# Kernel optimization log

Hardware: AMD Instinct MI355X
Metric: run time of the kernel (lower is better)

## Reference

```python
import jax, jax.numpy as jnp
import numpy as np

DIM_X, DIM_Y, BATCH = 64, 64, 2


def setup_inputs() -> dict:
    key = jax.random.key(0)
    k1, k2, k3 = jax.random.split(key, 3)
    mean_in = jax.random.normal(k1, (BATCH, DIM_X, DIM_Y), dtype=jnp.float32)
    # std must be positive
    std_in = jax.random.uniform(k2, (BATCH, DIM_X, DIM_Y), dtype=jnp.float32, minval=0.1, maxval=1.0)
    # identity correlation matrix -> PSD covariance, valid sqrt/div downstream
    n = DIM_X * DIM_Y
    corr_in = jnp.broadcast_to(jnp.eye(n, dtype=jnp.float32), (BATCH, n, n))
    # kaiming_uniform_(a=sqrt(5)) on a (dx, dy) weight -> bound = 1/sqrt(dy)
    bound = 1.0 / np.sqrt(DIM_Y)
    weight = jax.random.uniform(k3, (DIM_X, DIM_Y), dtype=jnp.float32, minval=-bound, maxval=bound)
    return {"mean_in": mean_in, "std_in": std_in, "corr_in": corr_in, "weight": weight}


def reference(mean_in, std_in, corr_in, weight):
    B, dx, dy = mean_in.shape
    n = dx * dy
    # fft(fft(w, dim=0), dim=1) == 2D FFT
    wfft = jnp.fft.fft2(weight)  # (dx, dy) complex

    # covariance from std and corr: cov[b,i,j,k,l] = std[b,i,j] * corr[b,i,j,k,l] * std[b,k,l]
    corr = corr_in.reshape(B, dx, dy, dx, dy)
    cov = std_in[:, None, None, :, :] * corr * std_in[:, :, :, None, None]

    # mean path: circular 2D convolution via FFT
    mean_fft = jnp.fft.fft2(mean_in, axes=(1, 2))
    mean_out = jnp.real(jnp.fft.ifft2(wfft[None] * mean_fft, axes=(1, 2)))

    # covariance path: 4D FFT, broadcast multiply by wfft on both index pairs, 4D IFFT
    cov_f = jnp.fft.fftn(cov, axes=(1, 2, 3, 4))
    cov_f = wfft[None, None, None, :, :] * cov_f * wfft[None, :, :, None, None]
    cov_out = jnp.real(jnp.fft.ifftn(cov_f, axes=(1, 2, 3, 4)))
    cov_out = cov_out.reshape(B, n, n)

    # update_correlation: std = sqrt(diag(cov)); corr = cov / (std outer std)
    var = jnp.diagonal(cov_out, axis1=-2, axis2=-1)  # (B, n)
    std_out = jnp.sqrt(jnp.maximum(var, 1e-12))
    denom = std_out[:, :, None] * std_out[:, None, :]
    corr_out = cov_out / denom
    std_out = std_out.reshape(B, dx, dy)
    return mean_out, std_out, corr_out
```

## Files before the change

### kernel.cpp

```cpp
#include <hip/hip_runtime.h>
#include <math.h>

#define DXY   64
#define NN    4096
#define NB    2
#define CP    65

#define C16 0.9238795325112867f
#define S16 0.3826834323650898f
#define R22 0.7071067811865476f

__device__ __forceinline__ void cmul_ip(float2& a, float wr, float wi) {
    float t = a.x * wr - a.y * wi;
    a.y = a.x * wi + a.y * wr;
    a.x = t;
}

__device__ __forceinline__ void bf4(float2* y, int i0, int i1, int i2, int i3, int inv) {
    float2 a0 = y[i0], a1 = y[i1], a2 = y[i2], a3 = y[i3];
    float t0r = a0.x + a2.x, t0i = a0.y + a2.y;
    float t1r = a0.x - a2.x, t1i = a0.y - a2.y;
    float t2r = a1.x + a3.x, t2i = a1.y + a3.y;
    float dr  = a1.x - a3.x, di  = a1.y - a3.y;
    float t3r, t3i;
    if (inv) { t3r = -di; t3i = dr; } else { t3r = di; t3i = -dr; }
    y[i0] = make_float2(t0r + t2r, t0i + t2i);
    y[i1] = make_float2(t1r + t3r, t1i + t3i);
    y[i2] = make_float2(t0r - t2r, t0i - t2i);
    y[i3] = make_float2(t1r - t3r, t1i - t3i);
}

__device__ __forceinline__ void fft16_fwd(float2* y) {
    bf4(y, 0, 4, 8, 12, 0);
    bf4(y, 1, 5, 9, 13, 0);
    cmul_ip(y[5],  C16, -S16); cmul_ip(y[9],  R22, -R22); cmul_ip(y[13],  S16, -C16);
    bf4(y, 2, 6, 10, 14, 0);
    cmul_ip(y[6],  R22, -R22); cmul_ip(y[10], 0.f, -1.f); cmul_ip(y[14], -R22, -R22);
    bf4(y, 3, 7, 11, 15, 0);
    cmul_ip(y[7],  S16, -C16); cmul_ip(y[11], -R22, -R22); cmul_ip(y[15], -C16,  S16);
    bf4(y, 0, 1, 2, 3, 0); bf4(y, 4, 5, 6, 7, 0);
    bf4(y, 8, 9, 10, 11, 0); bf4(y, 12, 13, 14, 15, 0);
}

__device__ __forceinline__ void fft16_inv(float2* y) {
    bf4(y, 0, 1, 2, 3, 1); bf4(y, 4, 5, 6, 7, 1);
    bf4(y, 8, 9, 10, 11, 1); bf4(y, 12, 13, 14, 15, 1);
    cmul_ip(y[5],  C16,  S16); cmul_ip(y[9],  R22,  R22); cmul_ip(y[13],  S16,  C16);
    cmul_ip(y[6],  R22,  R22); cmul_ip(y[10], 0.f,  1.f); cmul_ip(y[14], -R22,  R22);
    cmul_ip(y[7],  S16,  C16); cmul_ip(y[11], -R22,  R22); cmul_ip(y[15], -C16, -S16);
    bf4(y, 0, 4, 8, 12, 1); bf4(y, 1, 5, 9, 13, 1);
    bf4(y, 2, 6, 10, 14, 1); bf4(y, 3, 7, 11, 15, 1);
}

template<int US, int NS, bool FUSEW>
__device__ void fwd_pass(float2* z, const float2* __restrict__ wf, int u, int k1,
                         float c1r, float c1i, float s2, float2 Wb)
{
    const int B = u * US;
    float2 y[16];
    float twr = 1.f, twi = 0.f;
#pragma unroll
    for (int n2 = 0; n2 < 16; ++n2) {
        float2 x0 = z[B + n2 * NS];
        float2 x1 = z[B + (n2 + 16) * NS];
        float2 x2 = z[B + (n2 + 32) * NS];
        float2 x3 = z[B + (n2 + 48) * NS];
        float er  = fmaf(s2, x2.x, x0.x), ei = fmaf(s2, x2.y, x0.y);
        float orr = fmaf(s2, x3.x, x1.x), oi = fmaf(s2, x3.y, x1.y);
        float br = er + c1r * orr - c1i * oi;
        float bi = ei + c1r * oi + c1i * orr;
        y[n2].x = twr * br - twi * bi;
        y[n2].y = twr * bi + twi * br;
        float t = twr * Wb.x - twi * Wb.y;
        twi = twr * Wb.y + twi * Wb.x;
        twr = t;
    }
    fft16_fwd(y);
    if (FUSEW) {
#pragma unroll
        for (int p = 0; p < 16; ++p) {
            float2 wv = wf[(16 * k1 + p) * 64 + u];
            cmul_ip(y[p], wv.x, wv.y);
        }
    }
    __syncthreads();
#pragma unroll
    for (int p = 0; p < 16; ++p) z[B + (16 * k1 + p) * NS] = y[p];
    __syncthreads();
}

template<int US, int NS>
__device__ void inv_pass(float2* z, int u, int k1,
                         float ci1r, float ci1i, float s2, float2 Wbc)
{
    const int B = u * US;
    float2 y[16];
#pragma unroll
    for (int p = 0; p < 16; ++p) y[p] = z[B + (16 * k1 + p) * NS];
    fft16_inv(y);
    float twr = 1.f, twi = 0.f;
#pragma unroll
    for (int n2 = 0; n2 < 16; ++n2) {
        cmul_ip(y[n2], twr, twi);
        float t = twr * Wbc.x - twi * Wbc.y;
        twi = twr * Wbc.y + twi * Wbc.x;
        twr = t;
    }
#pragma unroll
    for (int n2 = 0; n2 < 16; ++n2) z[B + (16 * k1 + n2) * NS] = y[n2];
    __syncthreads();
    float2 xx[16];
#pragma unroll
    for (int n2 = 0; n2 < 16; ++n2) {
        float2 h0 = z[B + n2 * NS];
        float2 h1 = z[B + (n2 + 16) * NS];
        float2 h2 = z[B + (n2 + 32) * NS];
        float2 h3 = z[B + (n2 + 48) * NS];
        float er  = fmaf(s2, h2.x, h0.x), ei = fmaf(s2, h2.y, h0.y);
        float orr = fmaf(s2, h3.x, h1.x), oi = fmaf(s2, h3.y, h1.y);
        xx[n2].x = er + ci1r * orr - ci1i * oi;
        xx[n2].y = ei + ci1r * oi + ci1i * orr;
    }
    __syncthreads();
#pragma unroll
    for (int n2 = 0; n2 < 16; ++n2) z[B + (16 * k1 + n2) * NS] = xx[n2];
    __syncthreads();
}

__global__ __launch_bounds__(256, 4)
void row_conv2_kernel(const float* __restrict__ in, float* __restrict__ out,
                      const float2* __restrict__ wfft_br,
                      const float* __restrict__ sstd, float* var_out)
{
    __shared__ float2 z[64 * CP];
    const int tid = threadIdx.x;
    const int u   = ((tid >> 6) << 4) | (tid & 15);
    const int k1  = (tid >> 4) & 3;
    const float c1r = (k1 == 0) ? 1.f : ((k1 == 2) ? -1.f : 0.f);
    const float c1i = (k1 == 1) ? -1.f : ((k1 == 3) ? 1.f : 0.f);
    const float s2  = (k1 & 1) ? -1.f : 1.f;
    const float ang = -0.09817477042468103f * (float)k1;
    const float2 Wb  = make_float2(cosf(ang), sinf(ang));
    const float2 Wbc = make_float2(Wb.x, -Wb.y);
    const float ci1r = c1r, ci1i = -c1i;

    const int row0 = 2 * blockIdx.x;
    const long long off0 = (long long)row0 * NN, off1 = off0 + NN;
    const int b   = row0 >> 12;
    const int rI0 = row0 & (NN - 1), rI1 = rI0 + 1;
    const float* sb = nullptr;
    float sI0 = 1.f, sI1 = 1.f;
    if (sstd) { sb = sstd + (long long)b * NN; sI0 = sb[rI0]; sI1 = sb[rI1]; }

    float4 a4[4], c4[4], s4[4];
#pragma unroll
    for (int i = 0; i < 4; ++i) {
        int p = (tid + 256 * i) * 4;
        a4[i] = *(const float4*)(in + off0 + p);
        c4[i] = *(const float4*)(in + off1 + p);
    }
    if (sb) {
#pragma unroll
        for (int i = 0; i < 4; ++i) {
            int p = (tid + 256 * i) * 4;
            s4[i] = *(const float4*)(sb + p);
        }
    }
#pragma unroll
    for (int i = 0; i < 4; ++i) {
        int p = (tid + 256 * i) * 4;
        int r = p >> 6, c = p & 63;
        float4 a = a4[i], cc = c4[i];
        if (sb) {
            float4 s = s4[i];
            a.x *= sI0 * s.x; a.y *= sI0 * s.y; a.z *= sI0 * s.z; a.w *= sI0 * s.w;
            cc.x *= sI1 * s.x; cc.y *= sI1 * s.y; cc.z *= sI1 * s.z; cc.w *= sI1 * s.w;
        }
        float2* zp = z + r * CP + c;
        zp[0] = make_float2(a.x, cc.x);
        zp[1] = make_float2(a.y, cc.y);
        zp[2] = make_float2(a.z, cc.z);
        zp[3] = make_float2(a.w, cc.w);
    }
    __syncthreads();

    fwd_pass<CP, 1, false>(z, nullptr,  u, k1, c1r, c1i, s2, Wb);
    fwd_pass<1, CP, true >(z, wfft_br,  u, k1, c1r, c1i, s2, Wb);
    inv_pass<1, CP>(z, u, k1, ci1r, ci1i, s2, Wbc);
    inv_pass<CP, 1>(z, u, k1, ci1r, ci1i, s2, Wbc);

    const float scale = 1.0f / 4096.0f;
#pragma unroll
    for (int i = 0; i < 4; ++i) {
        int idx = tid + 256 * i;
        int p = idx * 4;
        int r = p >> 6, c = p & 63;
        const float2* zp = z + r * CP + c;
        float4 a, cc;
        a.x = zp[0].x * scale; a.y = zp[1].x * scale;
        a.z = zp[2].x * scale; a.w = zp[3].x * scale;
        cc.x = zp[0].y * scale; cc.y = zp[1].y * scale;
        cc.z = zp[2].y * scale; cc.w = zp[3].y * scale;
        *(float4*)(out + off0 + p) = a;
        *(float4*)(out + off1 + p) = cc;
    }
    if (var_out && tid == 0) {
        var_out[row0]     = z[(rI0 >> 6) * CP + (rI0 & 63)].x * scale;
        var_out[row0 + 1] = z[(rI1 >> 6) * CP + (rI1 & 63)].y * scale;
    }
}

__global__ __launch_bounds__(256, 4)
void wfft_kernel(const float* __restrict__ w, float2* wfft_br)
{
    __shared__ float2 z[64 * CP];
    const int tid = threadIdx.x;
    const int u   = ((tid >> 6) << 4) | (tid & 15);
    const int k1  = (tid >> 4) & 3;
    const float c1r = (k1 == 0) ? 1.f : ((k1 == 2) ? -1.f : 0.f);
    const float c1i = (k1 == 1) ? -1.f : ((k1 == 3) ? 1.f : 0.f);
    const float s2  = (k1 & 1) ? -1.f : 1.f;
    const float ang = -0.09817477042468103f * (float)k1;
    const float2 Wb = make_float2(cosf(ang), sinf(ang));

#pragma unroll
    for (int i = 0; i < 16; ++i) {
        int p = tid + 256 * i;
        z[(p >> 6) * CP + (p & 63)] = make_float2(w[p], 0.f);
    }
    __syncthreads();
    fwd_pass<CP, 1, false>(z, nullptr, u, k1, c1r, c1i, s2, Wb);
    fwd_pass<1, CP, false>(z, nullptr, u, k1, c1r, c1i, s2, Wb);
#pragma unroll
    for (int i = 0; i < 16; ++i) {
        int p = tid + 256 * i;
        wfft_br[p] = z[(p >> 6) * CP + (p & 63)];
    }
}

__global__ __launch_bounds__(256, 4)
void transpose_inplace_kernel(float* data)
{
    int bx = blockIdx.x, by = blockIdx.y, b = blockIdx.z;
    if (by > bx) return;
    __shared__ float tA[64 * 65];
    __shared__ float tB[64 * 65];
    const int f  = threadIdx.x & 15;
    const int r0 = threadIdx.x >> 4;
    long long base = (long long)b * NN * NN;
    float* A  = data + base + (long long)(by * 64) * NN + bx * 64;
    float* Bt = data + base + (long long)(bx * 64) * NN + by * 64;
    if (bx == by) {
        float4 va[4];
#pragma unroll
        for (int it = 0; it < 4; ++it) {
            int r = r0 + 16 * it;
            va[it] = *(const float4*)(A + (long long)r * NN + 4 * f);
        }
#pragma unroll
        for (int it = 0; it < 4; ++it) {
            int r = r0 + 16 * it;
            tA[(4 * f + 0) * 65 + r] = va[it].x; tA[(4 * f + 1) * 65 + r] = va[it].y;
            tA[(4 * f + 2) * 65 + r] = va[it].z; tA[(4 * f + 3) * 65 + r] = va[it].w;
        }
        __syncthreads();
#pragma unroll
        for (int it = 0; it < 4; ++it) {
            int c = r0 + 16 * it;
            float4 v;
            v.x = tA[c * 65 + 4 * f + 0]; v.y = tA[c * 65 + 4 * f + 1];
            v.z = tA[c * 65 + 4 * f + 2]; v.w = tA[c * 65 + 4 * f + 3];
            *(float4*)(A + (long long)c * NN + 4 * f) = v;
        }
    } else {
        float4 va[4], wb[4];
#pragma unroll
        for (int it = 0; it < 4; ++it) {
            int r = r0 + 16 * it;
            va[it] = *(const float4*)(A  + (long long)r * NN + 4 * f);
            wb[it] = *(const float4*)(Bt + (long long)r * NN + 4 * f);
        }
#pragma unroll
        for (int it = 0; it < 4; ++it) {
            int r = r0 + 16 * it;
            tA[(4 * f + 0) * 65 + r] = va[it].x; tA[(4 * f + 1) * 65 + r] = va[it].y;
            tA[(4 * f + 2) * 65 + r] = va[it].z; tA[(4 * f + 3) * 65 + r] = va[it].w;
            tB[(4 * f + 0) * 65 + r] = wb[it].x; tB[(4 * f + 1) * 65 + r] = wb[it].y;
            tB[(4 * f + 2) * 65 + r] = wb[it].z; tB[(4 * f + 3) * 65 + r] = wb[it].w;
        }
        __syncthreads();
        float4 ov[4], ow[4];
#pragma unroll
        for (int it = 0; it < 4; ++it) {
            int c = r0 + 16 * it;
            ov[it].x = tB[c * 65 + 4 * f + 0]; ov[it].y = tB[c * 65 + 4 * f + 1];
            ov[it].z = tB[c * 65 + 4 * f + 2]; ov[it].w = tB[c * 65 + 4 * f + 3];
            ow[it].x = tA[c * 65 + 4 * f + 0]; ow[it].y = tA[c * 65 + 4 * f + 1];
            ow[it].z = tA[c * 65 + 4 * f + 2]; ow[it].w = tA[c * 65 + 4 * f + 3];
        }
#pragma unroll
        for (int it = 0; it < 4; ++it) {
            int c = r0 + 16 * it;
            *(float4*)(A  + (long long)c * NN + 4 * f) = ov[it];
            *(float4*)(Bt + (long long)c * NN + 4 * f) = ow[it];
        }
    }
}

__global__ __launch_bounds__(256)
void std_kernel(const float* __restrict__ var, float* std_out, float* rstd, int n)
{
    int i = blockIdx.x * 256 + threadIdx.x;
    if (i < n) {
        float s = sqrtf(fmaxf(var[i], 1e-12f));
        std_out[i] = s;
        rstd[i] = 1.0f / s;
    }
}

__global__ __launch_bounds__(256)
void normalize_kernel(float* data, const float* __restrict__ rstd)
{
    const int tid = threadIdx.x;
    const int al  = blockIdx.x;
    const int bb  = al >> 12, a = al & (NN - 1);
    const float* rs = rstd + (long long)bb * NN;
    const float ra = rs[a];
    float* row = data + (long long)al * NN;
    float4 v[4], rb[4];
#pragma unroll
    for (int i = 0; i < 4; ++i) {
        int c = tid * 4 + 1024 * i;
        v[i]  = *(float4*)(row + c);
        rb[i] = *(const float4*)(rs + c);
    }
#pragma unroll
    for (int i = 0; i < 4; ++i) {
        int c = tid * 4 + 1024 * i;
        float4 t = v[i];
        t.x *= ra * rb[i].x; t.y *= ra * rb[i].y;
        t.z *= ra * rb[i].z; t.w *= ra * rb[i].w;
        *(float4*)(row + c) = t;
    }
}

extern "C" void kernel_launch(void* const* d_in, const int* in_sizes, int n_in,
                              void* d_out, int out_size, void* d_ws, size_t ws_size,
                              hipStream_t stream)
{
    const float* mean_in = (const float*)d_in[0];
    const float* std_in  = (const float*)d_in[1];
    const float* corr_in = (const float*)d_in[2];
    const float* weight  = (const float*)d_in[3];

    float* out      = (float*)d_out;
    float* mean_out = out;
    float* std_out  = out + 8192;
    float* corr_out = out + 16384;

    float*  ws      = (float*)d_ws;
    float2* wfft_br = (float2*)ws;
    float*  var_ws  = ws + 8192;
    float*  rstd_ws = ws + 16384;

    wfft_kernel<<<1, 256, 0, stream>>>(weight, wfft_br);

    row_conv2_kernel<<<1, 256, 0, stream>>>(mean_in, mean_out, wfft_br,
                                            nullptr, nullptr);

    row_conv2_kernel<<<NB * NN / 2, 256, 0, stream>>>(corr_in, corr_out, wfft_br,
                                                      std_in, nullptr);

    dim3 tg(64, 64, NB);
    transpose_inplace_kernel<<<tg, 256, 0, stream>>>(corr_out);

    row_conv2_kernel<<<NB * NN / 2, 256, 0, stream>>>(corr_out, corr_out, wfft_br,
                                                      nullptr, var_ws);

    std_kernel<<<(NB * NN + 255) / 256, 256, 0, stream>>>(var_ws, std_out,
                                                          rstd_ws, NB * NN);

    normalize_kernel<<<NB * NN, 256, 0, stream>>>(corr_out, rstd_ws);
}
```

Measured before the change: 462.6 us.

## Compute variance diagonal in transpose, fuse normalization into second conv pass

The diagonal of the final covariance is now computed directly during the in-place transpose, as a circular dot product of each column with the weight, and accumulated with atomics into a pre-zeroed buffer. That lets std/rstd be computed before the second row convolution, which now applies the rstd scaling in its epilogue. The separate normalize kernel, and its full read-modify-write of the 128 MB correlation tensor, is removed. The last inverse FFT pass writes straight from registers to global memory, skipping a shared-memory round trip. This adds atomics, extra shared-memory reads in the transpose, and a memset.

```diff
diff --git a/kernel.cpp b/kernel.cpp
--- a/kernel.cpp
+++ b/kernel.cpp
@@ -127,10 +127,44 @@
     __syncthreads();
 }
 
+template<int US, int NS>
+__device__ void inv_pass_last(float2* z, float2* xx, int u, int k1,
+                              float ci1r, float ci1i, float s2, float2 Wbc)
+{
+    const int B = u * US;
+    float2 y[16];
+#pragma unroll
+    for (int p = 0; p < 16; ++p) y[p] = z[B + (16 * k1 + p) * NS];
+    fft16_inv(y);
+    float twr = 1.f, twi = 0.f;
+#pragma unroll
+    for (int n2 = 0; n2 < 16; ++n2) {
+        cmul_ip(y[n2], twr, twi);
+        float t = twr * Wbc.x - twi * Wbc.y;
+        twi = twr * Wbc.y + twi * Wbc.x;
+        twr = t;
+    }
+#pragma unroll
+    for (int n2 = 0; n2 < 16; ++n2) z[B + (16 * k1 + n2) * NS] = y[n2];
+    __syncthreads();
+#pragma unroll
+    for (int n2 = 0; n2 < 16; ++n2) {
+        float2 h0 = z[B + n2 * NS];
+        float2 h1 = z[B + (n2 + 16) * NS];
+        float2 h2 = z[B + (n2 + 32) * NS];
+        float2 h3 = z[B + (n2 + 48) * NS];
+        float er  = fmaf(s2, h2.x, h0.x), ei = fmaf(s2, h2.y, h0.y);
+        float orr = fmaf(s2, h3.x, h1.x), oi = fmaf(s2, h3.y, h1.y);
+        xx[n2].x = er + ci1r * orr - ci1i * oi;
+        xx[n2].y = ei + ci1r * oi + ci1i * orr;
+    }
+}
+
 __global__ __launch_bounds__(256, 4)
 void row_conv2_kernel(const float* __restrict__ in, float* __restrict__ out,
                       const float2* __restrict__ wfft_br,
-                      const float* __restrict__ sstd, float* var_out)
+                      const float* __restrict__ sstd,
+                      const float* __restrict__ rstd)
 {
     __shared__ float2 z[64 * CP];
     const int tid = threadIdx.x;
@@ -187,26 +221,33 @@
     fwd_pass<CP, 1, false>(z, nullptr,  u, k1, c1r, c1i, s2, Wb);
     fwd_pass<1, CP, true >(z, wfft_br,  u, k1, c1r, c1i, s2, Wb);
     inv_pass<1, CP>(z, u, k1, ci1r, ci1i, s2, Wbc);
-    inv_pass<CP, 1>(z, u, k1, ci1r, ci1i, s2, Wbc);
+    float2 xx[16];
+    inv_pass_last<CP, 1>(z, xx, u, k1, ci1r, ci1i, s2, Wbc);
 
     const float scale = 1.0f / 4096.0f;
-#pragma unroll
-    for (int i = 0; i < 4; ++i) {
-        int idx = tid + 256 * i;
-        int p = idx * 4;
-        int r = p >> 6, c = p & 63;
-        const float2* zp = z + r * CP + c;
-        float4 a, cc;
-        a.x = zp[0].x * scale; a.y = zp[1].x * scale;
-        a.z = zp[2].x * scale; a.w = zp[3].x * scale;
-        cc.x = zp[0].y * scale; cc.y = zp[1].y * scale;
-        cc.z = zp[2].y * scale; cc.w = zp[3].y * scale;
-        *(float4*)(out + off0 + p) = a;
-        *(float4*)(out + off1 + p) = cc;
-    }
-    if (var_out && tid == 0) {
-        var_out[row0]     = z[(rI0 >> 6) * CP + (rI0 & 63)].x * scale;
-        var_out[row0 + 1] = z[(rI1 >> 6) * CP + (rI1 & 63)].y * scale;
+    float s0 = scale, s1 = scale;
+    const float* rsb = nullptr;
+    if (rstd) {
+        rsb = rstd + (long long)b * NN;
+        s0 *= rsb[rI0];
+        s1 *= rsb[rI1];
+    }
+    const int pbase = 64 * u + 16 * k1;
+#pragma unroll
+    for (int j = 0; j < 4; ++j) {
+        int p = pbase + 4 * j;
+        float4 f0 = make_float4(xx[4*j+0].x, xx[4*j+1].x, xx[4*j+2].x, xx[4*j+3].x);
+        float4 f1 = make_float4(xx[4*j+0].y, xx[4*j+1].y, xx[4*j+2].y, xx[4*j+3].y);
+        if (rsb) {
+            float4 rc = *(const float4*)(rsb + p);
+            f0.x *= s0 * rc.x; f0.y *= s0 * rc.y; f0.z *= s0 * rc.z; f0.w *= s0 * rc.w;
+            f1.x *= s1 * rc.x; f1.y *= s1 * rc.y; f1.z *= s1 * rc.z; f1.w *= s1 * rc.w;
+        } else {
+            f0.x *= s0; f0.y *= s0; f0.z *= s0; f0.w *= s0;
+            f1.x *= s1; f1.y *= s1; f1.z *= s1; f1.w *= s1;
+        }
+        *(float4*)(out + off0 + p) = f0;
+        *(float4*)(out + off1 + p) = f1;
     }
 }
 
@@ -238,18 +279,28 @@
     }
 }
 
-__global__ __launch_bounds__(256, 4)
-void transpose_inplace_kernel(float* data)
+__global__ __launch_bounds__(256, 2)
+void transpose_inplace_kernel(float* data, const float* __restrict__ weight,
+                              float* __restrict__ var)
 {
     int bx = blockIdx.x, by = blockIdx.y, b = blockIdx.z;
     if (by > bx) return;
     __shared__ float tA[64 * 65];
     __shared__ float tB[64 * 65];
-    const int f  = threadIdx.x & 15;
-    const int r0 = threadIdx.x >> 4;
+    __shared__ float wAs[64], wBs[64];
+    __shared__ float red[512];
+    const int tid = threadIdx.x;
+    const int f  = tid & 15;
+    const int r0 = tid >> 4;
     long long base = (long long)b * NN * NN;
     float* A  = data + base + (long long)(by * 64) * NN + bx * 64;
     float* Bt = data + base + (long long)(bx * 64) * NN + by * 64;
+
+    if (tid < 64)       wAs[tid]      = weight[(((bx - by) & 63) << 6) + tid];
+    else if (tid < 128) wBs[tid - 64] = weight[(((by - bx) & 63) << 6) + (tid - 64)];
+
+    const int c = tid & 63, q = tid >> 6;
+
     if (bx == by) {
         float4 va[4];
 #pragma unroll
@@ -264,13 +315,29 @@
             tA[(4 * f + 2) * 65 + r] = va[it].z; tA[(4 * f + 3) * 65 + r] = va[it].w;
         }
         __syncthreads();
-#pragma unroll
-        for (int it = 0; it < 4; ++it) {
-            int c = r0 + 16 * it;
-            float4 v;
-            v.x = tA[c * 65 + 4 * f + 0]; v.y = tA[c * 65 + 4 * f + 1];
-            v.z = tA[c * 65 + 4 * f + 2]; v.w = tA[c * 65 + 4 * f + 3];
-            *(float4*)(A + (long long)c * NN + 4 * f) = v;
+        float4 ov[4];
+#pragma unroll
+        for (int it = 0; it < 4; ++it) {
+            int cc = r0 + 16 * it;
+            ov[it].x = tA[cc * 65 + 4 * f + 0]; ov[it].y = tA[cc * 65 + 4 * f + 1];
+            ov[it].z = tA[cc * 65 + 4 * f + 2]; ov[it].w = tA[cc * 65 + 4 * f + 3];
+        }
+        float sA = 0.f;
+#pragma unroll
+        for (int k = 0; k < 16; ++k) {
+            int r = q * 16 + k;
+            sA = fmaf(wAs[(c - r) & 63], tA[c * 65 + r], sA);
+        }
+        red[tid] = sA;
+        __syncthreads();
+        if (tid < 64) {
+            float v = red[tid] + red[tid + 64] + red[tid + 128] + red[tid + 192];
+            atomicAdd(&var[(long long)b * NN + bx * 64 + tid], v);
+        }
+#pragma unroll
+        for (int it = 0; it < 4; ++it) {
+            int cc = r0 + 16 * it;
+            *(float4*)(A + (long long)cc * NN + 4 * f) = ov[it];
         }
     } else {
         float4 va[4], wb[4];
@@ -292,17 +359,34 @@
         float4 ov[4], ow[4];
 #pragma unroll
         for (int it = 0; it < 4; ++it) {
-            int c = r0 + 16 * it;
-            ov[it].x = tB[c * 65 + 4 * f + 0]; ov[it].y = tB[c * 65 + 4 * f + 1];
-            ov[it].z = tB[c * 65 + 4 * f + 2]; ov[it].w = tB[c * 65 + 4 * f + 3];
-            ow[it].x = tA[c * 65 + 4 * f + 0]; ow[it].y = tA[c * 65 + 4 * f + 1];
-            ow[it].z = tA[c * 65 + 4 * f + 2]; ow[it].w = tA[c * 65 + 4 * f + 3];
-        }
-#pragma unroll
-        for (int it = 0; it < 4; ++it) {
-            int c = r0 + 16 * it;
-            *(float4*)(A  + (long long)c * NN + 4 * f) = ov[it];
-            *(float4*)(Bt + (long long)c * NN + 4 * f) = ow[it];
+            int cc = r0 + 16 * it;
+            ov[it].x = tB[cc * 65 + 4 * f + 0]; ov[it].y = tB[cc * 65 + 4 * f + 1];
+            ov[it].z = tB[cc * 65 + 4 * f + 2]; ov[it].w = tB[cc * 65 + 4 * f + 3];
+            ow[it].x = tA[cc * 65 + 4 * f + 0]; ow[it].y = tA[cc * 65 + 4 * f + 1];
+            ow[it].z = tA[cc * 65 + 4 * f + 2]; ow[it].w = tA[cc * 65 + 4 * f + 3];
+        }
+        float sA = 0.f, sB = 0.f;
+#pragma unroll
+        for (int k = 0; k < 16; ++k) {
+            int r = q * 16 + k;
+            sA = fmaf(wAs[(c - r) & 63], tA[c * 65 + r], sA);
+            sB = fmaf(wBs[(c - r) & 63], tB[c * 65 + r], sB);
+        }
+        red[tid] = sA; red[256 + tid] = sB;
+        __syncthreads();
+        if (tid < 64) {
+            float v = red[tid] + red[tid + 64] + red[tid + 128] + red[tid + 192];
+            atomicAdd(&var[(long long)b * NN + bx * 64 + tid], v);
+        } else if (tid < 128) {
+            int t = tid - 64;
+            float v = red[256 + t] + red[320 + t] + red[384 + t] + red[448 + t];
+            atomicAdd(&var[(long long)b * NN + by * 64 + t], v);
+        }
+#pragma unroll
+        for (int it = 0; it < 4; ++it) {
+            int cc = r0 + 16 * it;
+            *(float4*)(A  + (long long)cc * NN + 4 * f) = ov[it];
+            *(float4*)(Bt + (long long)cc * NN + 4 * f) = ow[it];
         }
     }
 }
@@ -318,32 +402,6 @@
     }
 }
 
-__global__ __launch_bounds__(256)
-void normalize_kernel(float* data, const float* __restrict__ rstd)
-{
-    const int tid = threadIdx.x;
-    const int al  = blockIdx.x;
-    const int bb  = al >> 12, a = al & (NN - 1);
-    const float* rs = rstd + (long long)bb * NN;
-    const float ra = rs[a];
-    float* row = data + (long long)al * NN;
-    float4 v[4], rb[4];
-#pragma unroll
-    for (int i = 0; i < 4; ++i) {
-        int c = tid * 4 + 1024 * i;
-        v[i]  = *(float4*)(row + c);
-        rb[i] = *(const float4*)(rs + c);
-    }
-#pragma unroll
-    for (int i = 0; i < 4; ++i) {
-        int c = tid * 4 + 1024 * i;
-        float4 t = v[i];
-        t.x *= ra * rb[i].x; t.y *= ra * rb[i].y;
-        t.z *= ra * rb[i].z; t.w *= ra * rb[i].w;
-        *(float4*)(row + c) = t;
-    }
-}
-
 extern "C" void kernel_launch(void* const* d_in, const int* in_sizes, int n_in,
                               void* d_out, int out_size, void* d_ws, size_t ws_size,
                               hipStream_t stream)
@@ -363,6 +421,8 @@
     float*  var_ws  = ws + 8192;
     float*  rstd_ws = ws + 16384;
 
+    hipMemsetAsync(var_ws, 0, NB * NN * sizeof(float), stream);
+
     wfft_kernel<<<1, 256, 0, stream>>>(weight, wfft_br);
 
     row_conv2_kernel<<<1, 256, 0, stream>>>(mean_in, mean_out, wfft_br,
@@ -372,13 +432,11 @@
                                                       std_in, nullptr);
 
     dim3 tg(64, 64, NB);
-    transpose_inplace_kernel<<<tg, 256, 0, stream>>>(corr_out);
-
-    row_conv2_kernel<<<NB * NN / 2, 256, 0, stream>>>(corr_out, corr_out, wfft_br,
-                                                      nullptr, var_ws);
+    transpose_inplace_kernel<<<tg, 256, 0, stream>>>(corr_out, weight, var_ws);
 
     std_kernel<<<(NB * NN + 255) / 256, 256, 0, stream>>>(var_ws, std_out,
                                                           rstd_ws, NB * NN);
 
-    normalize_kernel<<<NB * NN, 256, 0, stream>>>(corr_out, rstd_ws);
-}
+    row_conv2_kernel<<<NB * NN / 2, 256, 0, stream>>>(corr_out, corr_out, wfft_br,
+                                                      nullptr, rstd_ws);
+}
```

Result: slower. 546.1 us (+18.0%).
